# Optimization experiments

Hardware: AMD Instinct MI355X
Metric: run time of the kernel (lower is better)

The kernel has to match this reference:

```python
import jax, jax.numpy as jnp
import numpy as np

N, F, R, H, C = 16384, 128, 16, 8, 64
E = 163840
SELF_LOOP_FILL = 0.5
NEG_SLOPE = 0.2


def _glorot(key, shape):
    fan = shape[0] + shape[-1]
    lim = jnp.sqrt(6.0 / fan)
    return jax.random.uniform(key, shape, jnp.float32, -lim, lim)


def setup_inputs() -> dict:
    key = jax.random.key(0)
    ks = jax.random.split(key, 20)
    inp = {
        'x': jax.random.normal(ks[0], (N, F), jnp.float32),
        'edge_index': jax.random.randint(ks[1], (2, E), 0, N, jnp.int64),
        'edge_attr': jax.random.uniform(ks[2], (E, R), jnp.float32),
        # layer 1 (concat=True): in=F, out per head=C, heads=H
        'Wl1': _glorot(ks[3], (F, H * C)), 'bl1': jnp.zeros((H * C,), jnp.float32),
        'Wr1': _glorot(ks[4], (F, H * C)), 'br1': jnp.zeros((H * C,), jnp.float32),
        'We1': _glorot(ks[5], (R, H * C)),
        'att1': _glorot(ks[6], (H, C)),
        'bias1': jnp.zeros((H * C,), jnp.float32),
        # layer 2 (concat=False): in=H*C
        'Wl2': _glorot(ks[7], (H * C, H * C)), 'bl2': jnp.zeros((H * C,), jnp.float32),
        'Wr2': _glorot(ks[8], (H * C, H * C)), 'br2': jnp.zeros((H * C,), jnp.float32),
        'We2': _glorot(ks[9], (R, H * C)),
        'att2': _glorot(ks[10], (H, C)),
        'bias2': jnp.zeros((C,), jnp.float32),
    }
    return inp


def gatv2_layer(x, src, dst, e, Wl, bl, Wr, br, We, att, bias, concat):
    n = x.shape[0]
    h, c = att.shape
    xl = (x @ Wl + bl).reshape(n, h, c)   # source transform (used for messages)
    xr = (x @ Wr + br).reshape(n, h, c)   # target transform
    ep = (e @ We).reshape(-1, h, c)       # edge feature transform [E',H,C]
    z = jax.nn.leaky_relu(xl[src] + xr[dst] + ep, NEG_SLOPE)  # [E',H,C]
    logits = jnp.einsum('ehc,hc->eh', z, att)                 # [E',H]
    # softmax over incoming edges of each destination node
    m = jax.ops.segment_max(logits, dst, num_segments=n)
    m = jax.lax.stop_gradient(jnp.where(jnp.isfinite(m), m, 0.0))
    ex = jnp.exp(logits - m[dst])
    denom = jax.ops.segment_sum(ex, dst, num_segments=n)
    alpha = ex / (denom[dst] + 1e-16)                         # [E',H]
    out = jax.ops.segment_sum(xl[src] * alpha[..., None], dst, num_segments=n)  # [N,H,C]
    out = out.reshape(n, h * c) if concat else out.mean(axis=1)
    return out + bias


def reference(x, edge_index, edge_attr, Wl1, bl1, Wr1, br1, We1, att1, bias1,
              Wl2, bl2, Wr2, br2, We2, att2, bias2):
    n = x.shape[0]
    loops = jnp.arange(n, dtype=edge_index.dtype)
    src = jnp.concatenate([edge_index[0], loops])
    dst = jnp.concatenate([edge_index[1], loops])
    e = jnp.concatenate([edge_attr, jnp.full((n, edge_attr.shape[1]), SELF_LOOP_FILL, edge_attr.dtype)])
    out = gatv2_layer(x, src, dst, e, Wl1, bl1, Wr1, br1, We1, att1, bias1, concat=True)
    out = gatv2_layer(out, src, dst, e, Wl2, bl2, Wr2, br2, We2, att2, bias2, concat=False)
    return out
```

## Files before the change

### kernel.cpp

```cpp
#include <hip/hip_runtime.h>
#include <cstdint>

#define NN 16384
#define FF 128
#define RR 16
#define HH 8
#define CC 64
#define HC 512
#define NC 1024
#define EE 163840
#define ET (EE + NN)

typedef __attribute__((ext_vector_type(2))) float f32x2;
typedef __attribute__((ext_vector_type(4))) float f32x4;
typedef __attribute__((ext_vector_type(8))) short short8;

__device__ __forceinline__ unsigned short f2bf(float f) {
  unsigned u = __builtin_bit_cast(unsigned, f);
  u = (u + 0x7FFFu + ((u >> 16) & 1u)) >> 16;
  return (unsigned short)u;
}
__device__ __forceinline__ float bf2f(unsigned short b) {
  unsigned u = ((unsigned)b) << 16;
  return __builtin_bit_cast(float, u);
}
__device__ __forceinline__ unsigned short f2h(float f) {
  return __builtin_bit_cast(unsigned short, (_Float16)f);
}
__device__ __forceinline__ float h2f(unsigned short h) {
  return (float)__builtin_bit_cast(_Float16, h);
}

__device__ __forceinline__ void gl_lds16(const void* g, void* l) {
  __builtin_amdgcn_global_load_lds(
      (const __attribute__((address_space(1))) unsigned int*)g,
      (__attribute__((address_space(3))) unsigned int*)l, 16, 0, 0);
}

__global__ __launch_bounds__(256) void count_kernel(const int* __restrict__ ei,
                                                    int* __restrict__ counts) {
  int e = blockIdx.x * 256 + threadIdx.x;
  if (e >= ET) return;
  int d = (e < EE) ? ei[EE + e] : (e - EE);
  atomicAdd(&counts[d], 1);
}

__global__ __launch_bounds__(1024) void scan_kernel(const int* __restrict__ counts,
                                                    int* __restrict__ offs,
                                                    int* __restrict__ cursor) {
  __shared__ int part[1024];
  int t = threadIdx.x;
  int base = t * 16;
  int loc[16];
  int s = 0;
#pragma unroll
  for (int i = 0; i < 16; ++i) { loc[i] = s; s += counts[base + i]; }
  part[t] = s;
  __syncthreads();
  for (int off = 1; off < 1024; off <<= 1) {
    int v = (t >= off) ? part[t - off] : 0;
    __syncthreads();
    part[t] += v;
    __syncthreads();
  }
  int excl = part[t] - s;
#pragma unroll
  for (int i = 0; i < 16; ++i) {
    int o = excl + loc[i];
    offs[base + i] = o;
    cursor[base + i] = o;
  }
  if (t == 1023) offs[NN] = part[1023];
}

__global__ __launch_bounds__(256) void scatter_kernel(const int* __restrict__ ei,
                                                      int* __restrict__ cursor,
                                                      int2* __restrict__ esrc) {
  int e = blockIdx.x * 256 + threadIdx.x;
  if (e >= ET) return;
  int s, d;
  if (e < EE) { s = ei[e]; d = ei[EE + e]; }
  else        { s = d = e - EE; }
  int p = atomicAdd(&cursor[d], 1);
  esrc[p] = make_int2(e, s);
}

__global__ __launch_bounds__(256) void pack_a_kernel(const float* __restrict__ A,
                                                     unsigned short* __restrict__ Ah,
                                                     unsigned short* __restrict__ Al,
                                                     int K) {
  int nkb = K >> 5;
  int rb = blockIdx.x / nkb, kb = blockIdx.x % nkb;
  int t = threadIdx.x;
  size_t obase = ((size_t)rb * nkb + kb) * 4096;
#pragma unroll
  for (int u = 0; u < 2; ++u) {
    int lin = t + u * 256;
    int r = lin >> 2, ch = lin & 3;
    int chs = (ch + (r >> 1)) & 3;
    const float* src = &A[(size_t)(rb * 128 + r) * K + kb * 32 + ch * 8];
    float4 v0 = *(const float4*)src;
    float4 v1 = *(const float4*)(src + 4);
    float v[8] = {v0.x, v0.y, v0.z, v0.w, v1.x, v1.y, v1.z, v1.w};
    short8 hv, lv;
#pragma unroll
    for (int j = 0; j < 8; ++j) {
      unsigned short h = f2bf(v[j]);
      unsigned short l = f2bf(v[j] - bf2f(h));
      hv[j] = (short)h; lv[j] = (short)l;
    }
    size_t o = obase + (size_t)r * 32 + chs * 8;
    *(short8*)&Ah[o] = hv;
    *(short8*)&Al[o] = lv;
  }
}

__global__ __launch_bounds__(256) void pack_w_kernel(const float* __restrict__ Wl,
                                                     const float* __restrict__ Wr,
                                                     unsigned short* __restrict__ Bh,
                                                     unsigned short* __restrict__ Bl,
                                                     int K) {
  int nkb = K >> 5;
  int nb = blockIdx.x / nkb, kb = blockIdx.x % nkb;
  int t = threadIdx.x;
  size_t obase = ((size_t)nb * nkb + kb) * 4096;
#pragma unroll
  for (int u = 0; u < 2; ++u) {
    int lin = t + u * 256;
    int n = lin >> 2, ch = lin & 3;
    int chs = (ch + (n >> 1)) & 3;
    int gn = nb * 128 + n;
    const float* W = (gn < HC) ? Wl : Wr;
    int cn = gn & (HC - 1);
    short8 hv, lv;
#pragma unroll
    for (int j = 0; j < 8; ++j) {
      float f = W[(size_t)(kb * 32 + ch * 8 + j) * HC + cn];
      unsigned short h = f2bf(f);
      unsigned short l = f2bf(f - bf2f(h));
      hv[j] = (short)h; lv[j] = (short)l;
    }
    size_t o = obase + (size_t)n * 32 + chs * 8;
    *(short8*)&Bh[o] = hv;
    *(short8*)&Bl[o] = lv;
  }
}

__global__ __launch_bounds__(256) void pack_wet_kernel(const float* __restrict__ We,
                                                       float* __restrict__ WeT) {
  int i = blockIdx.x * 256 + threadIdx.x;
  int c = i >> 4, r = i & 15;
  WeT[i] = We[r * HC + c];
}

__global__ __launch_bounds__(256) void gemm_mfma_kernel(const unsigned short* __restrict__ Ah,
                                                        const unsigned short* __restrict__ Al,
                                                        const unsigned short* __restrict__ Bh,
                                                        const unsigned short* __restrict__ Bl,
                                                        const float* __restrict__ bl,
                                                        const float* __restrict__ br,
                                                        float* __restrict__ C,
                                                        unsigned short* __restrict__ Chh,
                                                        int K) {
  __shared__ unsigned short lAh[4096], lAl[4096], lBh[4096], lBl[4096];
  int tid = threadIdx.x;
  int wave = tid >> 6, lane = tid & 63;
  int l15 = lane & 15, quad = lane >> 4;
  int wm = wave >> 1, wn = wave & 1;
  int nb = blockIdx.x, rb = blockIdx.y;
  int nkb = K >> 5;

  const unsigned short* src = (wave == 0) ? Ah : (wave == 1) ? Al : (wave == 2) ? Bh : Bl;
  unsigned short* dst = (wave == 0) ? lAh : (wave == 1) ? lAl : (wave == 2) ? lBh : lBl;
  int blk = (wave < 2) ? rb : nb;
  size_t gstep = 4096;
  const unsigned short* gbase = src + ((size_t)blk * nkb) * gstep + lane * 8;

  f32x4 acc[4][4];
#pragma unroll
  for (int i = 0; i < 4; ++i)
#pragma unroll
    for (int j = 0; j < 4; ++j) acc[i][j] = (f32x4){0.f, 0.f, 0.f, 0.f};

  int offA[4], offB[4];
#pragma unroll
  for (int t = 0; t < 4; ++t) {
    int ra = wm * 64 + t * 16 + l15;
    offA[t] = ra * 32 + ((quad + (ra >> 1)) & 3) * 8;
    int rbn = wn * 64 + t * 16 + l15;
    offB[t] = rbn * 32 + ((quad + (rbn >> 1)) & 3) * 8;
  }

  for (int kb = 0; kb < nkb; ++kb) {
    const unsigned short* g = gbase + (size_t)kb * gstep;
#pragma unroll
    for (int i = 0; i < 8; ++i)
      gl_lds16(g + i * 512, dst + i * 512);
    __syncthreads();

    short8 ah[4], al_[4], bh[4], bl_[4];
#pragma unroll
    for (int t = 0; t < 4; ++t) {
      ah[t]  = *(const short8*)&lAh[offA[t]];
      al_[t] = *(const short8*)&lAl[offA[t]];
      bh[t]  = *(const short8*)&lBh[offB[t]];
      bl_[t] = *(const short8*)&lBl[offB[t]];
    }
#pragma unroll
    for (int tm = 0; tm < 4; ++tm)
#pragma unroll
      for (int tn = 0; tn < 4; ++tn) {
        acc[tm][tn] = __builtin_amdgcn_mfma_f32_16x16x32_bf16(ah[tm], bh[tn], acc[tm][tn], 0, 0, 0);
        acc[tm][tn] = __builtin_amdgcn_mfma_f32_16x16x32_bf16(ah[tm], bl_[tn], acc[tm][tn], 0, 0, 0);
        acc[tm][tn] = __builtin_amdgcn_mfma_f32_16x16x32_bf16(al_[tm], bh[tn], acc[tm][tn], 0, 0, 0);
      }
    __syncthreads();
  }

#pragma unroll
  for (int tm = 0; tm < 4; ++tm) {
    int row = rb * 128 + wm * 64 + tm * 16 + quad * 4;
#pragma unroll
    for (int tn = 0; tn < 4; ++tn) {
      int col = nb * 128 + wn * 64 + tn * 16 + l15;
      bool xlh_half = (col < HC);
      float bias = xlh_half ? bl[col] : br[col - HC];
#pragma unroll
      for (int r = 0; r < 4; ++r) {
        float v = acc[tm][tn][r] + bias;
        if (xlh_half)
          Chh[(size_t)(row + r) * HC + col] = f2h(v);
        else
          C[(size_t)(row + r) * NC + col] = v;
      }
    }
  }
}


__device__ __forceinline__ void fused_edge_body(
    const int2* __restrict__ esrc,
    const int* __restrict__ offs, const float* __restrict__ eattr,
    const float* __restrict__ WeT, const float* __restrict__ att,
    const float* __restrict__ xlr, const unsigned short* __restrict__ xlh,
    int n, int t, float& out0, float& out1) {
  int c0 = t * 2;
  int beg = offs[n], end = offs[n + 1];
  f32x2 wf0[8], wf1[8];
  {
    const f32x2* w0 = (const f32x2*)&WeT[(size_t)c0 * RR];
    const f32x2* w1 = (const f32x2*)&WeT[(size_t)(c0 + 1) * RR];
#pragma unroll
    for (int j = 0; j < 8; ++j) { wf0[j] = w0[j]; wf1[j] = w1[j]; }
  }
  float2 amv = *(const float2*)&att[c0];
  f32x2 rv = *(const f32x2*)&xlr[(size_t)n * NC + HC + c0];
  float m = -1e30f, l = 0.f;
  f32x2 acc = (f32x2){0.f, 0.f};
#pragma unroll 2
  for (int i = beg; i < end; ++i) {
    int2 es = esrc[i];
    int e = es.x, s = es.y;
    unsigned lu = *(const unsigned*)&xlh[(size_t)s * HC + c0];
    f32x2 lv = (f32x2){h2f((unsigned short)(lu & 0xFFFFu)),
                       h2f((unsigned short)(lu >> 16))};
    f32x4 ea0, ea1, ea2, ea3;
    if (e < EE) {
      const f32x4* ep4 = (const f32x4*)&eattr[(size_t)e * RR];
      ea0 = ep4[0]; ea1 = ep4[1]; ea2 = ep4[2]; ea3 = ep4[3];
    } else {
      ea0 = ea1 = ea2 = ea3 = (f32x4){0.5f, 0.5f, 0.5f, 0.5f};
    }
    f32x2 er[8];
    er[0] = __builtin_shufflevector(ea0, ea0, 0, 1);
    er[1] = __builtin_shufflevector(ea0, ea0, 2, 3);
    er[2] = __builtin_shufflevector(ea1, ea1, 0, 1);
    er[3] = __builtin_shufflevector(ea1, ea1, 2, 3);
    er[4] = __builtin_shufflevector(ea2, ea2, 0, 1);
    er[5] = __builtin_shufflevector(ea2, ea2, 2, 3);
    er[6] = __builtin_shufflevector(ea3, ea3, 0, 1);
    er[7] = __builtin_shufflevector(ea3, ea3, 2, 3);
    f32x2 epp0 = (f32x2){0.f, 0.f};
    f32x2 epp1 = (f32x2){0.f, 0.f};
#pragma unroll
    for (int j = 0; j < 8; ++j) {
      epp0 = __builtin_elementwise_fma(er[j], wf0[j], epp0);
      epp1 = __builtin_elementwise_fma(er[j], wf1[j], epp1);
    }
    f32x2 base2 = lv + rv;
    float z0 = base2.x + (epp0.x + epp0.y);
    float z1 = base2.y + (epp1.x + epp1.y);
    z0 = fmaf(0.2f, fminf(z0, 0.f), fmaxf(z0, 0.f));
    z1 = fmaf(0.2f, fminf(z1, 0.f), fmaxf(z1, 0.f));
    float p = fmaf(z0, amv.x, z1 * amv.y);
    p += __shfl_xor(p, 1);
    p += __shfl_xor(p, 2);
    p += __shfl_xor(p, 4);
    p += __shfl_xor(p, 8);
    p += __shfl_xor(p, 16);
    float nm = fmaxf(m, p);
    float sc = __expf(m - nm);
    float el = __expf(p - nm);
    l = l * sc + el;
    acc.x = acc.x * sc + el * lv.x;
    acc.y = acc.y * sc + el * lv.y;
    m = nm;
  }
  float inv = 1.f / (l + 1e-16f);
  out0 = acc.x * inv;
  out1 = acc.y * inv;
}

__global__ __launch_bounds__(256) void fused_concat_kernel(
    const int2* __restrict__ esrc,
    const int* __restrict__ offs, const float* __restrict__ eattr,
    const float* __restrict__ WeT, const float* __restrict__ att,
    const float* __restrict__ xlr, const unsigned short* __restrict__ xlh,
    const float* __restrict__ bias,
    unsigned short* __restrict__ Ah2, unsigned short* __restrict__ Al2) {
  int n = blockIdx.x, t = threadIdx.x;
  float o0, o1;
  fused_edge_body(esrc, offs, eattr, WeT, att, xlr, xlh, n, t, o0, o1);
  int c0 = t * 2;
  float v0 = o0 + bias[c0];
  float v1 = o1 + bias[c0 + 1];
  int r = n & 127, rbk = n >> 7;
#pragma unroll
  for (int u = 0; u < 2; ++u) {
    int c = c0 + u;
    float v = u ? v1 : v0;
    int kb = c >> 5, ch = (c >> 3) & 3, j = c & 7;
    int chs = (ch + (r >> 1)) & 3;
    size_t idx = ((size_t)rbk * 16 + kb) * 4096 + (size_t)r * 32 + chs * 8 + j;
    unsigned short h = f2bf(v);
    Ah2[idx] = h;
    Al2[idx] = f2bf(v - bf2f(h));
  }
}

__global__ __launch_bounds__(256) void fused_mean_kernel(
    const int2* __restrict__ esrc,
    const int* __restrict__ offs, const float* __restrict__ eattr,
    const float* __restrict__ WeT, const float* __restrict__ att,
    const float* __restrict__ xlr, const unsigned short* __restrict__ xlh,
    const float* __restrict__ bias2, float* __restrict__ out) {
  __shared__ float red[HC];
  int n = blockIdx.x, t = threadIdx.x;
  float o0, o1;
  fused_edge_body(esrc, offs, eattr, WeT, att, xlr, xlh, n, t, o0, o1);
  int c0 = t * 2;
  red[c0] = o0;
  red[c0 + 1] = o1;
  __syncthreads();
  if (t < CC) {
    float ssum = 0.f;
#pragma unroll
    for (int hh = 0; hh < HH; ++hh) ssum += red[hh * CC + t];
    out[(size_t)n * CC + t] = ssum * 0.125f + bias2[t];
  }
}

extern "C" void kernel_launch(void* const* d_in, const int* in_sizes, int n_in,
                              void* d_out, int out_size, void* d_ws, size_t ws_size,
                              hipStream_t stream) {
  const float* x     = (const float*)d_in[0];
  const int*   ei    = (const int*)d_in[1];
  const float* eattr = (const float*)d_in[2];
  const float* Wl1   = (const float*)d_in[3];
  const float* bl1   = (const float*)d_in[4];
  const float* Wr1   = (const float*)d_in[5];
  const float* br1   = (const float*)d_in[6];
  const float* We1   = (const float*)d_in[7];
  const float* att1  = (const float*)d_in[8];
  const float* bias1 = (const float*)d_in[9];
  const float* Wl2   = (const float*)d_in[10];
  const float* bl2   = (const float*)d_in[11];
  const float* Wr2   = (const float*)d_in[12];
  const float* br2   = (const float*)d_in[13];
  const float* We2   = (const float*)d_in[14];
  const float* att2  = (const float*)d_in[15];
  const float* bias2 = (const float*)d_in[16];
  float* out = (float*)d_out;

  char* ws = (char*)d_ws;
  size_t off = 0;
  auto alloc = [&](size_t bytes) {
    char* p = ws + off;
    off += (bytes + 255) & ~(size_t)255;
    return p;
  };
  float* bufC = (float*)alloc((size_t)NN * NC * 4);
  unsigned short* xlh = (unsigned short*)alloc((size_t)NN * HC * 2);
  unsigned short* Ah1 = (unsigned short*)alloc((size_t)NN * FF * 2);
  unsigned short* Al1 = (unsigned short*)alloc((size_t)NN * FF * 2);
  unsigned short* Ah2 = (unsigned short*)alloc((size_t)NN * HC * 2);
  unsigned short* Al2 = (unsigned short*)alloc((size_t)NN * HC * 2);
  unsigned short* Wh1 = (unsigned short*)alloc((size_t)FF * NC * 2);
  unsigned short* Wlo1 = (unsigned short*)alloc((size_t)FF * NC * 2);
  unsigned short* Wh2 = (unsigned short*)alloc((size_t)HC * NC * 2);
  unsigned short* Wlo2 = (unsigned short*)alloc((size_t)HC * NC * 2);
  float* WeT1 = (float*)alloc((size_t)HC * RR * 4);
  float* WeT2 = (float*)alloc((size_t)HC * RR * 4);
  int* counts = (int*)alloc((size_t)NN * 4);
  int* offs   = (int*)alloc((size_t)(NN + 1) * 4);
  int* cursor = (int*)alloc((size_t)NN * 4);
  int2* esrc  = (int2*)alloc((size_t)ET * 8);
  (void)ws_size; (void)in_sizes; (void)n_in; (void)out_size;

  hipMemsetAsync(counts, 0, (size_t)NN * 4, stream);
  int eb = (ET + 255) / 256;
  count_kernel<<<eb, 256, 0, stream>>>(ei, counts);
  scan_kernel<<<1, 1024, 0, stream>>>(counts, offs, cursor);
  scatter_kernel<<<eb, 256, 0, stream>>>(ei, cursor, esrc);

  pack_a_kernel<<<(NN / 128) * (FF / 32), 256, 0, stream>>>(x, Ah1, Al1, FF);
  pack_w_kernel<<<(NC / 128) * (FF / 32), 256, 0, stream>>>(Wl1, Wr1, Wh1, Wlo1, FF);
  pack_w_kernel<<<(NC / 128) * (HC / 32), 256, 0, stream>>>(Wl2, Wr2, Wh2, Wlo2, HC);
  pack_wet_kernel<<<(HC * RR) / 256, 256, 0, stream>>>(We1, WeT1);
  pack_wet_kernel<<<(HC * RR) / 256, 256, 0, stream>>>(We2, WeT2);

  dim3 ggrid(NC / 128, NN / 128);

  gemm_mfma_kernel<<<ggrid, 256, 0, stream>>>(Ah1, Al1, Wh1, Wlo1, bl1, br1, bufC, xlh, FF);
  fused_concat_kernel<<<NN, 256, 0, stream>>>(esrc, offs, eattr, WeT1, att1, bufC, xlh, bias1, Ah2, Al2);

  gemm_mfma_kernel<<<ggrid, 256, 0, stream>>>(Ah2, Al2, Wh2, Wlo2, bl2, br2, bufC, xlh, HC);
  fused_mean_kernel<<<NN, 256, 0, stream>>>(esrc, offs, eattr, WeT2, att2, bufC, xlh, bias2, out);
}
```

Baseline: 479.2 us.

## Process two nodes per block with four channels per thread in edge kernels

Measured after the change: 566.2 us. +18.1%, slower.

```diff
diff --git a/kernel.cpp b/kernel.cpp
--- a/kernel.cpp
+++ b/kernel.cpp
@@ -238,32 +238,36 @@
 }
 
 
-__device__ __forceinline__ void fused_edge_body(
+__device__ __forceinline__ f32x4 lrelu4(f32x4 z) {
+  f32x4 zn = __builtin_elementwise_min(z, (f32x4){0.f, 0.f, 0.f, 0.f});
+  f32x4 zp = __builtin_elementwise_max(z, (f32x4){0.f, 0.f, 0.f, 0.f});
+  return __builtin_elementwise_fma((f32x4){0.2f, 0.2f, 0.2f, 0.2f}, zn, zp);
+}
+
+__device__ __forceinline__ void fused_edge_body4(
     const int2* __restrict__ esrc,
     const int* __restrict__ offs, const float* __restrict__ eattr,
     const float* __restrict__ WeT, const float* __restrict__ att,
     const float* __restrict__ xlr, const unsigned short* __restrict__ xlh,
-    int n, int t, float& out0, float& out1) {
-  int c0 = t * 2;
+    int n, int tt , f32x4& outv) {
+  int c0 = tt * 4;
   int beg = offs[n], end = offs[n + 1];
-  f32x2 wf0[8], wf1[8];
+  f32x4 w[16];
   {
-    const f32x2* w0 = (const f32x2*)&WeT[(size_t)c0 * RR];
-    const f32x2* w1 = (const f32x2*)&WeT[(size_t)(c0 + 1) * RR];
-#pragma unroll
-    for (int j = 0; j < 8; ++j) { wf0[j] = w0[j]; wf1[j] = w1[j]; }
-  }
-  float2 amv = *(const float2*)&att[c0];
-  f32x2 rv = *(const f32x2*)&xlr[(size_t)n * NC + HC + c0];
+    const f32x4* wp = (const f32x4*)&WeT[(size_t)c0 * RR];
+#pragma unroll
+    for (int k = 0; k < 16; ++k) w[k] = wp[k];
+  }
+  f32x4 amv = *(const f32x4*)&att[c0];
+  f32x4 rv  = *(const f32x4*)&xlr[(size_t)n * NC + HC + c0];
   float m = -1e30f, l = 0.f;
-  f32x2 acc = (f32x2){0.f, 0.f};
+  f32x4 acc = (f32x4){0.f, 0.f, 0.f, 0.f};
 #pragma unroll 2
   for (int i = beg; i < end; ++i) {
     int2 es = esrc[i];
     int e = es.x, s = es.y;
-    unsigned lu = *(const unsigned*)&xlh[(size_t)s * HC + c0];
-    f32x2 lv = (f32x2){h2f((unsigned short)(lu & 0xFFFFu)),
-                       h2f((unsigned short)(lu >> 16))};
+    ushort4 lu = *(const ushort4*)&xlh[(size_t)s * HC + c0];
+    f32x4 lv = (f32x4){h2f(lu.x), h2f(lu.y), h2f(lu.z), h2f(lu.w)};
     f32x4 ea0, ea1, ea2, ea3;
     if (e < EE) {
       const f32x4* ep4 = (const f32x4*)&eattr[(size_t)e * RR];
@@ -271,44 +275,45 @@
     } else {
       ea0 = ea1 = ea2 = ea3 = (f32x4){0.5f, 0.5f, 0.5f, 0.5f};
     }
-    f32x2 er[8];
-    er[0] = __builtin_shufflevector(ea0, ea0, 0, 1);
-    er[1] = __builtin_shufflevector(ea0, ea0, 2, 3);
-    er[2] = __builtin_shufflevector(ea1, ea1, 0, 1);
-    er[3] = __builtin_shufflevector(ea1, ea1, 2, 3);
-    er[4] = __builtin_shufflevector(ea2, ea2, 0, 1);
-    er[5] = __builtin_shufflevector(ea2, ea2, 2, 3);
-    er[6] = __builtin_shufflevector(ea3, ea3, 0, 1);
-    er[7] = __builtin_shufflevector(ea3, ea3, 2, 3);
-    f32x2 epp0 = (f32x2){0.f, 0.f};
-    f32x2 epp1 = (f32x2){0.f, 0.f};
-#pragma unroll
-    for (int j = 0; j < 8; ++j) {
-      epp0 = __builtin_elementwise_fma(er[j], wf0[j], epp0);
-      epp1 = __builtin_elementwise_fma(er[j], wf1[j], epp1);
-    }
-    f32x2 base2 = lv + rv;
-    float z0 = base2.x + (epp0.x + epp0.y);
-    float z1 = base2.y + (epp1.x + epp1.y);
-    z0 = fmaf(0.2f, fminf(z0, 0.f), fmaxf(z0, 0.f));
-    z1 = fmaf(0.2f, fminf(z1, 0.f), fmaxf(z1, 0.f));
-    float p = fmaf(z0, amv.x, z1 * amv.y);
+    f32x4 q0 = (f32x4){0.f, 0.f, 0.f, 0.f};
+    f32x4 q1 = q0, q2 = q0, q3 = q0;
+    q0 = __builtin_elementwise_fma(ea0, w[0],  q0);
+    q0 = __builtin_elementwise_fma(ea1, w[1],  q0);
+    q0 = __builtin_elementwise_fma(ea2, w[2],  q0);
+    q0 = __builtin_elementwise_fma(ea3, w[3],  q0);
+    q1 = __builtin_elementwise_fma(ea0, w[4],  q1);
+    q1 = __builtin_elementwise_fma(ea1, w[5],  q1);
+    q1 = __builtin_elementwise_fma(ea2, w[6],  q1);
+    q1 = __builtin_elementwise_fma(ea3, w[7],  q1);
+    q2 = __builtin_elementwise_fma(ea0, w[8],  q2);
+    q2 = __builtin_elementwise_fma(ea1, w[9],  q2);
+    q2 = __builtin_elementwise_fma(ea2, w[10], q2);
+    q2 = __builtin_elementwise_fma(ea3, w[11], q2);
+    q3 = __builtin_elementwise_fma(ea0, w[12], q3);
+    q3 = __builtin_elementwise_fma(ea1, w[13], q3);
+    q3 = __builtin_elementwise_fma(ea2, w[14], q3);
+    q3 = __builtin_elementwise_fma(ea3, w[15], q3);
+    f32x4 ep = (f32x4){(q0.x + q0.y) + (q0.z + q0.w),
+                       (q1.x + q1.y) + (q1.z + q1.w),
+                       (q2.x + q2.y) + (q2.z + q2.w),
+                       (q3.x + q3.y) + (q3.z + q3.w)};
+    f32x4 z = lrelu4(lv + rv + ep);
+    float p = fmaf(z.x, amv.x, fmaf(z.y, amv.y, fmaf(z.z, amv.z, z.w * amv.w)));
     p += __shfl_xor(p, 1);
     p += __shfl_xor(p, 2);
     p += __shfl_xor(p, 4);
     p += __shfl_xor(p, 8);
-    p += __shfl_xor(p, 16);
     float nm = fmaxf(m, p);
     float sc = __expf(m - nm);
     float el = __expf(p - nm);
     l = l * sc + el;
-    acc.x = acc.x * sc + el * lv.x;
-    acc.y = acc.y * sc + el * lv.y;
+    f32x4 scv = (f32x4){sc, sc, sc, sc};
+    f32x4 elv = (f32x4){el, el, el, el};
+    acc = __builtin_elementwise_fma(acc, scv, elv * lv);
     m = nm;
   }
   float inv = 1.f / (l + 1e-16f);
-  out0 = acc.x * inv;
-  out1 = acc.y * inv;
+  outv = acc * (f32x4){inv, inv, inv, inv};
 }
 
 __global__ __launch_bounds__(256) void fused_concat_kernel(
@@ -318,17 +323,18 @@
     const float* __restrict__ xlr, const unsigned short* __restrict__ xlh,
     const float* __restrict__ bias,
     unsigned short* __restrict__ Ah2, unsigned short* __restrict__ Al2) {
-  int n = blockIdx.x, t = threadIdx.x;
-  float o0, o1;
-  fused_edge_body(esrc, offs, eattr, WeT, att, xlr, xlh, n, t, o0, o1);
-  int c0 = t * 2;
-  float v0 = o0 + bias[c0];
-  float v1 = o1 + bias[c0 + 1];
+  int t = threadIdx.x;
+  int half = t >> 7, tt = t & 127;
+  int n = blockIdx.x * 2 + half;
+  f32x4 o;
+  fused_edge_body4(esrc, offs, eattr, WeT, att, xlr, xlh, n, tt, o);
+  int c0 = tt * 4;
   int r = n & 127, rbk = n >> 7;
-#pragma unroll
-  for (int u = 0; u < 2; ++u) {
+  float ov[4] = {o.x, o.y, o.z, o.w};
+#pragma unroll
+  for (int u = 0; u < 4; ++u) {
     int c = c0 + u;
-    float v = u ? v1 : v0;
+    float v = ov[u] + bias[c];
     int kb = c >> 5, ch = (c >> 3) & 3, j = c & 7;
     int chs = (ch + (r >> 1)) & 3;
     size_t idx = ((size_t)rbk * 16 + kb) * 4096 + (size_t)r * 32 + chs * 8 + j;
@@ -344,19 +350,20 @@
     const float* __restrict__ WeT, const float* __restrict__ att,
     const float* __restrict__ xlr, const unsigned short* __restrict__ xlh,
     const float* __restrict__ bias2, float* __restrict__ out) {
-  __shared__ float red[HC];
-  int n = blockIdx.x, t = threadIdx.x;
-  float o0, o1;
-  fused_edge_body(esrc, offs, eattr, WeT, att, xlr, xlh, n, t, o0, o1);
-  int c0 = t * 2;
-  red[c0] = o0;
-  red[c0 + 1] = o1;
+  __shared__ float red[2][HC];
+  int t = threadIdx.x;
+  int half = t >> 7, tt = t & 127;
+  int n = blockIdx.x * 2 + half;
+  f32x4 o;
+  fused_edge_body4(esrc, offs, eattr, WeT, att, xlr, xlh, n, tt, o);
+  int c0 = tt * 4;
+  *(f32x4*)&red[half][c0] = o;
   __syncthreads();
-  if (t < CC) {
+  if (tt < CC) {
     float ssum = 0.f;
 #pragma unroll
-    for (int hh = 0; hh < HH; ++hh) ssum += red[hh * CC + t];
-    out[(size_t)n * CC + t] = ssum * 0.125f + bias2[t];
+    for (int hh = 0; hh < HH; ++hh) ssum += red[half][hh * CC + tt];
+    out[(size_t)n * CC + tt] = ssum * 0.125f + bias2[tt];
   }
 }
 
@@ -422,8 +429,8 @@
   dim3 ggrid(NC / 128, NN / 128);
 
   gemm_mfma_kernel<<<ggrid, 256, 0, stream>>>(Ah1, Al1, Wh1, Wlo1, bl1, br1, bufC, xlh, FF);
-  fused_concat_kernel<<<NN, 256, 0, stream>>>(esrc, offs, eattr, WeT1, att1, bufC, xlh, bias1, Ah2, Al2);
+  fused_concat_kernel<<<NN / 2, 256, 0, stream>>>(esrc, offs, eattr, WeT1, att1, bufC, xlh, bias1, Ah2, Al2);
 
   gemm_mfma_kernel<<<ggrid, 256, 0, stream>>>(Ah2, Al2, Wh2, Wlo2, bl2, br2, bufC, xlh, HC);
-  fused_mean_kernel<<<NN, 256, 0, stream>>>(esrc, offs, eattr, WeT2, att2, bufC, xlh, bias2, out);
-}
+  fused_mean_kernel<<<NN / 2, 256, 0, stream>>>(esrc, offs, eattr, WeT2, att2, bufC, xlh, bias2, out);
+}
```
